# Kernel optimization log

Hardware: AMD Instinct MI355X
Metric: run time of the kernel (lower is better)

## Reference

```python
import jax, jax.numpy as jnp
import numpy as np

N_QUBITS = 8
DIM = 1 << N_QUBITS  # 256
PI = float(np.pi)

# Computational-basis bit signs: s_i = +1 for bit 0, -1 for bit 1 (Z eigenvalues).
# PennyLane convention: wire 0 is the most-significant bit.
_bits = (np.arange(DIM)[:, None] >> (N_QUBITS - 1 - np.arange(N_QUBITS))[None, :]) & 1
SIGNS = jnp.asarray(1.0 - 2.0 * _bits, dtype=jnp.float32)  # [DIM, 8]
PAIR_SIGNS = SIGNS[:, :-1] * SIGNS[:, 1:]                  # [DIM, 7]


def _mlp(x, W1, b1, W2, b2, W3, b3):
    h = jax.nn.relu(x @ W1.T + b1)
    h = jax.nn.relu(h @ W2.T + b2)
    return h @ W3.T + b3


def _embed_state(x):
    """QuantumEmbedding1 (ZZ feature map, IQP-style) on |0>^8.

    H on every wire, RZ(x_i) on wire i, then for i in 0..6:
    CNOT(i,i+1); RZ((pi-x_i)(pi-x_{i+1}), wire i+1); CNOT(i,i+1).
    The whole post-Hadamard circuit is diagonal, so the statevector has
    closed form: psi_b = 2^{-4} exp(-i/2 * phi(b)).
    x: [B, 8] -> psi: [B, 256] complex64.
    """
    single = x @ SIGNS.T                                    # [B, DIM]
    zz = (PI - x[:, :-1]) * (PI - x[:, 1:])                 # [B, 7]
    phase = single + zz @ PAIR_SIGNS.T                      # [B, DIM]
    return jnp.exp(-0.5j * phase) / 16.0                    # complex64


def _mean_rho(psi):
    B = psi.shape[0]
    return jnp.einsum('bi,bj->ij', psi, jnp.conj(psi)) / B  # [256, 256]


def setup_inputs() -> dict:
    key = jax.random.key(0)
    ks = jax.random.split(key, 8)
    B = 65536
    inp = {
        'x1': jax.random.normal(ks[0], (B, 8), dtype=jnp.float32),
        'x0': jax.random.normal(ks[1], (B, 8), dtype=jnp.float32),
        'W1': jax.random.normal(ks[2], (10, 8), dtype=jnp.float32) / np.sqrt(8.0),
        'b1': jnp.zeros((10,), dtype=jnp.float32),
        'W2': jax.random.normal(ks[3], (10, 10), dtype=jnp.float32) / np.sqrt(10.0),
        'b2': jnp.zeros((10,), dtype=jnp.float32),
        'W3': jax.random.normal(ks[4], (8, 10), dtype=jnp.float32) / np.sqrt(10.0),
        'b3': jnp.zeros((8,), dtype=jnp.float32),
    }
    return inp


def reference(x1, x0, W1, b1, W2, b2, W3, b3):
    h1 = _mlp(x1, W1, b1, W2, b2, W3, b3)
    h0 = _mlp(x0, W1, b1, W2, b2, W3, b3)
    rho1 = _mean_rho(_embed_state(h1))
    rho0 = _mean_rho(_embed_state(h0))
    rho_diff = rho1 - rho0
    rho_diff = 0.5 * (rho_diff + jnp.conj(rho_diff.T))  # exact Hermitian
    eigvals = jnp.linalg.eigvalsh(rho_diff)             # real eigenvalues
    return -0.5 * jnp.sum(jnp.abs(eigvals))
```

## Files before the change

kernel.cpp:

```cpp
#include <hip/hip_runtime.h>
#include <cstdint>
#include <cstddef>
#include <utility>

#define PI_F 3.14159265358979323846f

typedef __attribute__((ext_vector_type(8))) _Float16 half8;
typedef __attribute__((ext_vector_type(4))) float f32x4;

struct U4 { unsigned int w[4]; };

static __device__ __forceinline__ unsigned int packhalf2(float c, float s) {
  _Float16 hc = (_Float16)c, hs = (_Float16)s;
  unsigned short uc = __builtin_bit_cast(unsigned short, hc);
  unsigned short us = __builtin_bit_cast(unsigned short, hs);
  return (unsigned int)uc | ((unsigned int)us << 16);
}

static __device__ __forceinline__ void load16_lds(const void* g, void* l) {
  __builtin_amdgcn_global_load_lds(
      (const __attribute__((address_space(1))) unsigned int*)g,
      (__attribute__((address_space(3))) unsigned int*)l, 16, 0, 0);
}

__global__ __launch_bounds__(256) void k_gen(
    const float* __restrict__ x1, const float* __restrict__ x0,
    const float* __restrict__ W1, const float* __restrict__ b1,
    const float* __restrict__ W2, const float* __restrict__ b2,
    const float* __restrict__ W3, const float* __restrict__ b3, int B,
    _Float16* __restrict__ Ach, float* __restrict__ scalars,
    float* __restrict__ out) {
  __shared__ float hzl[32][17];
  int kb = blockIdx.x, t = threadIdx.x;
  if (kb == 0 && t == 0) {
    scalars[0] = 0.f;
    scalars[1] = 0.f;
    out[0] = 0.f;
  }
  if (t < 32) {
    int smp = kb * 32 + t;
    const float* xp =
        (smp < B) ? (x1 + (size_t)smp * 8) : (x0 + (size_t)(smp - B) * 8);
    float x[8];
#pragma unroll
    for (int k = 0; k < 8; k++) x[k] = xp[k];
    float a1[10];
#pragma unroll
    for (int o = 0; o < 10; o++) {
      float v = b1[o];
#pragma unroll
      for (int k = 0; k < 8; k++) v = fmaf(W1[o * 8 + k], x[k], v);
      a1[o] = fmaxf(v, 0.f);
    }
    float a2[10];
#pragma unroll
    for (int o = 0; o < 10; o++) {
      float v = b2[o];
#pragma unroll
      for (int k = 0; k < 10; k++) v = fmaf(W2[o * 10 + k], a1[k], v);
      a2[o] = fmaxf(v, 0.f);
    }
    float hh[8];
#pragma unroll
    for (int o = 0; o < 8; o++) {
      float v = b3[o];
#pragma unroll
      for (int k = 0; k < 10; k++) v = fmaf(W3[o * 10 + k], a2[k], v);
      hh[o] = v;
    }
#pragma unroll
    for (int k = 0; k < 8; k++) hzl[t][k] = hh[k];
#pragma unroll
    for (int k = 0; k < 7; k++)
      hzl[t][8 + k] = (PI_F - hh[k]) * (PI_F - hh[k + 1]);
  }
  __syncthreads();
  int s = t & 31, oct = t >> 5;
  float h[8], z[7];
#pragma unroll
  for (int k = 0; k < 8; k++) h[k] = hzl[s][k];
#pragma unroll
  for (int k = 0; k < 7; k++) z[k] = hzl[s][8 + k];
  float S5 = (oct & 4) ? -1.f : 1.f;
  float S6 = (oct & 2) ? -1.f : 1.f;
  float S7 = (oct & 1) ? -1.f : 1.f;
  float sg[5] = {1.f, 1.f, 1.f, 1.f, 1.f};
  float phi = h[0] + h[1] + h[2] + h[3] + h[4] + S5 * h[5] + S6 * h[6] +
              S7 * h[7] + z[0] + z[1] + z[2] + z[3] + S5 * z[4] +
              S5 * S6 * z[5] + S6 * S7 * z[6];
  _Float16* dst = Ach + (size_t)kb * 16384;
  const int halfoff = (2 * s) ^ (oct << 3);

  auto emit = [&](int g, float ph) {
    float r = ph * 0.07957747154594767f;
    r = r - floorf(r);
    float sv = __builtin_amdgcn_sinf(r);
    float cv = __builtin_amdgcn_cosf(r);
    *(unsigned int*)(dst + (size_t)(g * 8 + oct) * 64 + halfoff) =
        packhalf2(cv, sv);
  };

  emit(0, phi);
#pragma unroll
  for (int jj = 1; jj < 32; ++jj) {
    const int b = __builtin_ctz(jj);
    const int w = 4 - b;
    float nbl = (w == 0) ? 0.f : sg[w - 1] * z[w - 1];
    float nbr = (w == 4) ? S5 * z[4] : sg[w + 1] * z[w];
    phi -= 2.f * sg[w] * (h[w] + nbl + nbr);
    sg[w] = -sg[w];
    emit(jj ^ (jj >> 1), phi);
  }
}

__global__ __launch_bounds__(512) void k_gemm_q(const _Float16* __restrict__ A,
                                                float* __restrict__ P) {
  __shared__ _Float16 lds[2][16384];
  int b = blockIdx.x;
  int qt = (b < 128) ? 0 : (b < 384 ? 1 : 2);
  int z = b - ((qt == 0) ? 0 : (qt == 1) ? 128 : 384);
  int kbPer = (qt == 1) ? 16 : 32;
  int kb0 = z * kbPer;
  int chunkOff = (qt == 2) ? 16384 : 0;
  int bRowBase = (qt == 1) ? 128 : 0;
  int t = threadIdx.x, wave = t >> 6, lane = t & 63;
  unsigned int reMask = (kb0 < 2048) ? 0u : 0x80008000u;
  unsigned int imMask = (kb0 < 2048) ? 0x80000000u : 0x00008000u;

  auto stage = [&](int it, int buf) {
    const char* g = (const char*)A + (size_t)(kb0 + it) * 32768 + chunkOff;
    char* l = (char*)&lds[buf][0];
    load16_lds(g + t * 16, l + t * 16);
    load16_lds(g + 8192 + t * 16, l + 8192 + t * 16);
    if (qt == 1) {
      load16_lds(g + 16384 + t * 16, l + 16384 + t * 16);
      load16_lds(g + 24576 + t * 16, l + 24576 + t * 16);
    }
  };

  f32x4 accR[2][4] = {};
  f32x4 accI[2][4] = {};
  stage(0, 0);
  for (int it = 0; it < kbPer; ++it) {
    __syncthreads();
    if (it + 1 < kbPer) stage(it + 1, (it + 1) & 1);
    int buf = it & 1;
#pragma unroll
    for (int kk = 0; kk < 2; kk++) {
      int cb = kk * 4 + (lane >> 4);
      half8 af[2];
#pragma unroll
      for (int fr = 0; fr < 2; fr++) {
        int r = (wave >> 1) * 32 + fr * 16 + (lane & 15);
        af[fr] = *(const half8*)&lds[buf][r * 64 + ((cb ^ (r & 7)) << 3)];
      }
#pragma unroll
      for (int fc = 0; fc < 4; fc++) {
        int rb = bRowBase + (wave & 1) * 64 + fc * 16 + (lane & 15);
        half8 bv = *(const half8*)&lds[buf][rb * 64 + ((cb ^ (rb & 7)) << 3)];
        U4 u = __builtin_bit_cast(U4, bv), ur, ui;
#pragma unroll
        for (int q = 0; q < 4; q++) {
          unsigned int xv = u.w[q];
          ur.w[q] = xv ^ reMask;
          ui.w[q] = ((xv << 16) | (xv >> 16)) ^ imMask;
        }
        half8 bfr = __builtin_bit_cast(half8, ur);
        half8 bfi = __builtin_bit_cast(half8, ui);
#pragma unroll
        for (int fr = 0; fr < 2; fr++) {
          accR[fr][fc] = __builtin_amdgcn_mfma_f32_16x16x32_f16(
              af[fr], bfr, accR[fr][fc], 0, 0, 0);
          accI[fr][fc] = __builtin_amdgcn_mfma_f32_16x16x32_f16(
              af[fr], bfi, accI[fr][fc], 0, 0, 0);
        }
      }
    }
  }
  float* PR = P + (size_t)b * 32768;
  float* PI = PR + 16384;
  int r4 = (lane >> 4) * 4, cj = lane & 15;
#pragma unroll
  for (int fr = 0; fr < 2; fr++)
#pragma unroll
    for (int fc = 0; fc < 4; fc++)
#pragma unroll
      for (int r = 0; r < 4; r++) {
        int li = (wave >> 1) * 32 + fr * 16 + r4 + r;
        int lj = (wave & 1) * 64 + fc * 16 + cj;
        PR[li * 128 + lj] = accR[fr][fc][r];
        PI[li * 128 + lj] = accI[fr][fc][r];
      }
}

__global__ __launch_bounds__(128) void k_reduce1(const float* __restrict__ P,
                                                 float* __restrict__ Q) {
  int r = blockIdx.x, qt = blockIdx.y, g = blockIdx.z, c = threadIdx.x;
  int nsl = (qt == 1) ? 32 : 16;
  int b0 = ((qt == 0) ? 0 : (qt == 1) ? 128 : 384) + g * nsl;
  float vR = 0.f, vI = 0.f;
  for (int u = 0; u < nsl; u++) {
    const float* base = P + (size_t)(b0 + u) * 32768 + r * 128 + c;
    vR += base[0];
    vI += base[16384];
  }
  size_t qidx = ((size_t)(g * 3 + qt) * 128 + r) * 128 + c;
  Q[qidx] = vR;
  Q[qidx + (size_t)8 * 3 * 16384] = vI;
}

__global__ __launch_bounds__(128) void k_reduce2(const float* __restrict__ Q,
                                                 float* __restrict__ AR,
                                                 float* __restrict__ AI,
                                                 float* __restrict__ sumsq,
                                                 float scale) {
  int r = blockIdx.x, qt = blockIdx.y, c = threadIdx.x;
  float vR = 0.f, vI = 0.f;
#pragma unroll
  for (int g = 0; g < 8; g++) {
    size_t qidx = ((size_t)(g * 3 + qt) * 128 + r) * 128 + c;
    vR += Q[qidx];
    vI += Q[qidx + (size_t)8 * 3 * 16384];
  }
  vR *= scale;
  vI *= scale;
  int i = (qt == 2) ? 128 + r : r;
  int j = (qt == 0) ? c : 128 + c;
  float ss = 0.f;
  bool diagQ = (qt != 1);
  if (!diagQ || c > r) {
    AR[i * 256 + j] = vR;
    AR[j * 256 + i] = vR;
    AI[i * 256 + j] = vI;
    AI[j * 256 + i] = -vI;
    ss = 2.f * (vR * vR + vI * vI);
  } else if (c == r) {
    AR[i * 256 + j] = vR;
    AI[i * 256 + j] = 0.f;
    ss = vR * vR;
  }
#pragma unroll
  for (int o = 32; o > 0; o >>= 1) ss += __shfl_down(ss, o);
  __shared__ float w2[2];
  if ((c & 63) == 0) w2[c >> 6] = ss;
  __syncthreads();
  if (c == 0) atomicAdd(sumsq, w2[0] + w2[1]);
}

__global__ __launch_bounds__(1024) void k_csq(
    const float* __restrict__ XR, const float* __restrict__ XI,
    float* __restrict__ YR, float* __restrict__ YI,
    float* __restrict__ sumsqY, int accumNorm) {
  __shared__ float rp[16][258][2];
  __shared__ float cpT[16][258][2];
  __shared__ float pacc[3][256][2];
  __shared__ float w16[16];
  int t = threadIdx.x;
  int bi = blockIdx.x >> 4, bj = blockIdx.x & 15;
  {
    int r = t >> 6, c = (t & 63) * 4;
    const float4 vr = *(const float4*)&XR[(bi * 16 + r) * 256 + c];
    const float4 vi = *(const float4*)&XI[(bi * 16 + r) * 256 + c];
    float4 p0 = {vr.x, vi.x, vr.y, vi.y};
    float4 p1 = {vr.z, vi.z, vr.w, vi.w};
    *(float4*)&rp[r][c][0] = p0;
    *(float4*)&rp[r][c + 2][0] = p1;
    int row = t >> 2, c0 = (t & 3) * 4;
    const float4 wr = *(const float4*)&XR[row * 256 + bj * 16 + c0];
    const float4 wi = *(const float4*)&XI[row * 256 + bj * 16 + c0];
    float2 q0 = {wr.x, wi.x}, q1 = {wr.y, wi.y};
    float2 q2 = {wr.z, wi.z}, q3 = {wr.w, wi.w};
    *(float2*)&cpT[c0 + 0][row][0] = q0;
    *(float2*)&cpT[c0 + 1][row][0] = q1;
    *(float2*)&cpT[c0 + 2][row][0] = q2;
    *(float2*)&cpT[c0 + 3][row][0] = q3;
  }
  __syncthreads();
  int sub = t >> 8, tt = t & 255, ty = tt >> 4, tx = tt & 15;
  float sR = 0.f, sI = 0.f;
  int k0 = sub * 64;
#pragma unroll 8
  for (int k = k0; k < k0 + 64; k++) {
    float xr = rp[ty][k][0], xi = rp[ty][k][1];
    float yr = cpT[tx][k][0], yi = cpT[tx][k][1];
    sR = fmaf(xr, yr, sR);
    sR = fmaf(-xi, yi, sR);
    sI = fmaf(xr, yi, sI);
    sI = fmaf(xi, yr, sI);
  }
  if (sub) {
    pacc[sub - 1][tt][0] = sR;
    pacc[sub - 1][tt][1] = sI;
  }
  __syncthreads();
  float v = 0.f;
  if (sub == 0) {
    sR += (pacc[0][tt][0] + pacc[1][tt][0]) + pacc[2][tt][0];
    sI += (pacc[0][tt][1] + pacc[1][tt][1]) + pacc[2][tt][1];
    int i = bi * 16 + ty, j = bj * 16 + tx;
    YR[i * 256 + j] = sR;
    YI[i * 256 + j] = sI;
    if (accumNorm) v = sR * sR + sI * sI;
  }
#pragma unroll
  for (int o = 32; o > 0; o >>= 1) v += __shfl_down(v, o);
  if ((t & 63) == 0) w16[t >> 6] = v;
  __syncthreads();
  if (t == 0 && accumNorm)
    atomicAdd(sumsqY, (w16[0] + w16[1]) + (w16[2] + w16[3]));
}

__global__ __launch_bounds__(1024) void k_cupd(
    const float* __restrict__ XR, const float* __restrict__ XI,
    const float* __restrict__ YR, const float* __restrict__ YI,
    float* __restrict__ ZR, float* __restrict__ ZI,
    const float* __restrict__ scalars, int mode,
    const float* __restrict__ AR, const float* __restrict__ AI,
    float* __restrict__ out, int finalTrace) {
  __shared__ float rp[16][258][2];
  __shared__ float cpT[16][258][2];
  __shared__ float pacc[3][256][2];
  __shared__ float w16[16];
  int t = threadIdx.x;
  int bi = blockIdx.x >> 4, bj = blockIdx.x & 15;
  {
    int r = t >> 6, c = (t & 63) * 4;
    const float4 vr = *(const float4*)&XR[(bi * 16 + r) * 256 + c];
    const float4 vi = *(const float4*)&XI[(bi * 16 + r) * 256 + c];
    float4 p0 = {vr.x, vi.x, vr.y, vi.y};
    float4 p1 = {vr.z, vi.z, vr.w, vi.w};
    *(float4*)&rp[r][c][0] = p0;
    *(float4*)&rp[r][c + 2][0] = p1;
    int row = t >> 2, c0 = (t & 3) * 4;
    const float4 wr = *(const float4*)&YR[row * 256 + bj * 16 + c0];
    const float4 wi = *(const float4*)&YI[row * 256 + bj * 16 + c0];
    float2 q0 = {wr.x, wi.x}, q1 = {wr.y, wi.y};
    float2 q2 = {wr.z, wi.z}, q3 = {wr.w, wi.w};
    *(float2*)&cpT[c0 + 0][row][0] = q0;
    *(float2*)&cpT[c0 + 1][row][0] = q1;
    *(float2*)&cpT[c0 + 2][row][0] = q2;
    *(float2*)&cpT[c0 + 3][row][0] = q3;
  }
  __syncthreads();
  int sub = t >> 8, tt = t & 255, ty = tt >> 4, tx = tt & 15;
  float sR = 0.f, sI = 0.f;
  int k0 = sub * 64;
#pragma unroll 8
  for (int k = k0; k < k0 + 64; k++) {
    float xr = rp[ty][k][0], xi = rp[ty][k][1];
    float yr = cpT[tx][k][0], yi = cpT[tx][k][1];
    sR = fmaf(xr, yr, sR);
    sR = fmaf(-xi, yi, sR);
    sI = fmaf(xr, yi, sI);
    sI = fmaf(xi, yr, sI);
  }
  if (sub) {
    pacc[sub - 1][tt][0] = sR;
    pacc[sub - 1][tt][1] = sI;
  }
  __syncthreads();
  float v = 0.f;
  if (sub == 0) {
    sR += (pacc[0][tt][0] + pacc[1][tt][0]) + pacc[2][tt][0];
    sI += (pacc[0][tt][1] + pacc[1][tt][1]) + pacc[2][tt][1];
    float aC, bC;
    if (mode == 0) {
      float f2 = scalars[0];
      float f = sqrtf(f2);
      float Rhat = 1.41421356f * sqrtf(scalars[1]) / f2;
      float g = 1.0f / (1.75f * Rhat);
      aC = 1.5f * g / f;
      float gf = g / f;
      bC = 0.5f * gf * gf * gf;
    } else if (mode == 1) {
      aC = 2.0f;
      bC = 1.0f;
    } else {
      aC = 1.5f;
      bC = 0.5f;
    }
    int idx = (bi * 16 + ty) * 256 + bj * 16 + tx;
    float zr = aC * XR[idx] - bC * sR;
    float zi = aC * XI[idx] - bC * sI;
    if (!finalTrace) {
      ZR[idx] = zr;
      ZI[idx] = zi;
    } else {
      v = AR[idx] * zr + AI[idx] * zi;
    }
  }
#pragma unroll
  for (int o = 32; o > 0; o >>= 1) v += __shfl_down(v, o);
  if ((t & 63) == 0) w16[t >> 6] = v;
  __syncthreads();
  if (t == 0 && finalTrace)
    atomicAdd(out, -0.5f * ((w16[0] + w16[1]) + (w16[2] + w16[3])));
}

extern "C" void kernel_launch(void* const* d_in, const int* in_sizes, int n_in,
                              void* d_out, int out_size, void* d_ws,
                              size_t ws_size, hipStream_t stream) {
  const float* x1 = (const float*)d_in[0];
  const float* x0 = (const float*)d_in[1];
  const float* W1 = (const float*)d_in[2];
  const float* b1 = (const float*)d_in[3];
  const float* W2 = (const float*)d_in[4];
  const float* b2 = (const float*)d_in[5];
  const float* W3 = (const float*)d_in[6];
  const float* b3 = (const float*)d_in[7];
  (void)n_in;
  (void)out_size;
  (void)ws_size;

  const int B = in_sizes[0] / 8;
  const int total = 2 * B;
  const int totalKb = total / 32;

  char* ws = (char*)d_ws;
  size_t off = 0;
  auto carve = [&](size_t bytes) -> void* {
    off = (off + 255) & ~(size_t)255;
    void* p = ws + off;
    off += bytes;
    return p;
  };
  _Float16* Ach = (_Float16*)carve((size_t)totalKb * 16384 * 2);
  float* P = (float*)carve((size_t)512 * 32768 * 4);
  float* Q = (float*)carve((size_t)2 * 8 * 3 * 16384 * 4);
  float* scalars = (float*)carve(256);
  float* AR = (float*)carve(256 * 256 * 4);
  float* AI = (float*)carve(256 * 256 * 4);
  float* XR = (float*)carve(256 * 256 * 4);
  float* XI = (float*)carve(256 * 256 * 4);
  float* YR = (float*)carve(256 * 256 * 4);
  float* YI = (float*)carve(256 * 256 * 4);
  float* ZR = (float*)carve(256 * 256 * 4);
  float* ZI = (float*)carve(256 * 256 * 4);

  k_gen<<<totalKb, 256, 0, stream>>>(x1, x0, W1, b1, W2, b2, W3, b3, B, Ach,
                                     scalars, (float*)d_out);
  k_gemm_q<<<512, 512, 0, stream>>>(Ach, P);
  k_reduce1<<<dim3(128, 3, 8), 128, 0, stream>>>(P, Q);
  k_reduce2<<<dim3(128, 3), 128, 0, stream>>>(Q, AR, AI, scalars,
                                              1.0f / (256.0f * (float)B));

  const int NIT = 11;
  float *cR = AR, *cI = AI, *nR = XR, *nI = XI;
  for (int it = 0; it < NIT; it++) {
    int mode = (it == 0) ? 0 : (it <= 6 ? 1 : 2);
    int fin = (it == NIT - 1) ? 1 : 0;
    k_csq<<<256, 1024, 0, stream>>>(cR, cI, YR, YI, scalars + 1, it == 0);
    k_cupd<<<256, 1024, 0, stream>>>(cR, cI, YR, YI, nR, nI, scalars, mode, AR,
                                     AI, (float*)d_out, fin);
    if (it == 0) {
      cR = XR; cI = XI; nR = ZR; nI = ZI;
    } else {
      std::swap(cR, nR);
      std::swap(cI, nI);
    }
  }
}
```

Measured before the change: 229.1 us.

## Fuse statevector phase generation into GEMM, staging only MLP features

The MLP now runs in its own kernel and writes 16 floats per sample, replacing the full fp16 statevector chunk (256 complex values per sample) that used to go to global memory. The GEMM kernel rebuilds the needed statevector rows directly in LDS with the Gray-code phase recurrence, overlapping this generation with the MFMA work on the other buffer. This removes a large global write and read of the statevector. In exchange the GEMM blocks take on sin/cos work, and generation is repeated for blocks that share rows.

```diff
diff --git a/kernel.cpp b/kernel.cpp
--- a/kernel.cpp
+++ b/kernel.cpp
@@ -17,133 +17,150 @@
   return (unsigned int)uc | ((unsigned int)us << 16);
 }
 
-static __device__ __forceinline__ void load16_lds(const void* g, void* l) {
-  __builtin_amdgcn_global_load_lds(
-      (const __attribute__((address_space(1))) unsigned int*)g,
-      (__attribute__((address_space(3))) unsigned int*)l, 16, 0, 0);
-}
-
-__global__ __launch_bounds__(256) void k_gen(
+__global__ __launch_bounds__(256) void k_mlp(
     const float* __restrict__ x1, const float* __restrict__ x0,
     const float* __restrict__ W1, const float* __restrict__ b1,
     const float* __restrict__ W2, const float* __restrict__ b2,
-    const float* __restrict__ W3, const float* __restrict__ b3, int B,
-    _Float16* __restrict__ Ach, float* __restrict__ scalars,
+    const float* __restrict__ W3, const float* __restrict__ b3,
+    float* __restrict__ hz, int B, float* __restrict__ scalars,
     float* __restrict__ out) {
-  __shared__ float hzl[32][17];
-  int kb = blockIdx.x, t = threadIdx.x;
-  if (kb == 0 && t == 0) {
+  int s = blockIdx.x * blockDim.x + threadIdx.x;
+  if (blockIdx.x == 0 && threadIdx.x == 0) {
     scalars[0] = 0.f;
     scalars[1] = 0.f;
     out[0] = 0.f;
   }
-  if (t < 32) {
-    int smp = kb * 32 + t;
-    const float* xp =
-        (smp < B) ? (x1 + (size_t)smp * 8) : (x0 + (size_t)(smp - B) * 8);
-    float x[8];
-#pragma unroll
-    for (int k = 0; k < 8; k++) x[k] = xp[k];
-    float a1[10];
-#pragma unroll
-    for (int o = 0; o < 10; o++) {
-      float v = b1[o];
-#pragma unroll
-      for (int k = 0; k < 8; k++) v = fmaf(W1[o * 8 + k], x[k], v);
-      a1[o] = fmaxf(v, 0.f);
-    }
-    float a2[10];
-#pragma unroll
-    for (int o = 0; o < 10; o++) {
-      float v = b2[o];
-#pragma unroll
-      for (int k = 0; k < 10; k++) v = fmaf(W2[o * 10 + k], a1[k], v);
-      a2[o] = fmaxf(v, 0.f);
-    }
-    float hh[8];
-#pragma unroll
-    for (int o = 0; o < 8; o++) {
-      float v = b3[o];
-#pragma unroll
-      for (int k = 0; k < 10; k++) v = fmaf(W3[o * 10 + k], a2[k], v);
-      hh[o] = v;
-    }
-#pragma unroll
-    for (int k = 0; k < 8; k++) hzl[t][k] = hh[k];
-#pragma unroll
-    for (int k = 0; k < 7; k++)
-      hzl[t][8 + k] = (PI_F - hh[k]) * (PI_F - hh[k + 1]);
-  }
-  __syncthreads();
-  int s = t & 31, oct = t >> 5;
-  float h[8], z[7];
-#pragma unroll
-  for (int k = 0; k < 8; k++) h[k] = hzl[s][k];
-#pragma unroll
-  for (int k = 0; k < 7; k++) z[k] = hzl[s][8 + k];
-  float S5 = (oct & 4) ? -1.f : 1.f;
-  float S6 = (oct & 2) ? -1.f : 1.f;
-  float S7 = (oct & 1) ? -1.f : 1.f;
-  float sg[5] = {1.f, 1.f, 1.f, 1.f, 1.f};
-  float phi = h[0] + h[1] + h[2] + h[3] + h[4] + S5 * h[5] + S6 * h[6] +
-              S7 * h[7] + z[0] + z[1] + z[2] + z[3] + S5 * z[4] +
-              S5 * S6 * z[5] + S6 * S7 * z[6];
-  _Float16* dst = Ach + (size_t)kb * 16384;
-  const int halfoff = (2 * s) ^ (oct << 3);
-
-  auto emit = [&](int g, float ph) {
-    float r = ph * 0.07957747154594767f;
-    r = r - floorf(r);
-    float sv = __builtin_amdgcn_sinf(r);
-    float cv = __builtin_amdgcn_cosf(r);
-    *(unsigned int*)(dst + (size_t)(g * 8 + oct) * 64 + halfoff) =
-        packhalf2(cv, sv);
-  };
-
-  emit(0, phi);
-#pragma unroll
-  for (int jj = 1; jj < 32; ++jj) {
-    const int b = __builtin_ctz(jj);
-    const int w = 4 - b;
-    float nbl = (w == 0) ? 0.f : sg[w - 1] * z[w - 1];
-    float nbr = (w == 4) ? S5 * z[4] : sg[w + 1] * z[w];
-    phi -= 2.f * sg[w] * (h[w] + nbl + nbr);
-    sg[w] = -sg[w];
-    emit(jj ^ (jj >> 1), phi);
-  }
-}
-
-__global__ __launch_bounds__(512) void k_gemm_q(const _Float16* __restrict__ A,
+  if (s >= 2 * B) return;
+  const float* xp = (s < B) ? (x1 + (size_t)s * 8) : (x0 + (size_t)(s - B) * 8);
+  float x[8];
+#pragma unroll
+  for (int k = 0; k < 8; k++) x[k] = xp[k];
+  float a1[10];
+#pragma unroll
+  for (int o = 0; o < 10; o++) {
+    float v = b1[o];
+#pragma unroll
+    for (int k = 0; k < 8; k++) v = fmaf(W1[o * 8 + k], x[k], v);
+    a1[o] = fmaxf(v, 0.f);
+  }
+  float a2[10];
+#pragma unroll
+  for (int o = 0; o < 10; o++) {
+    float v = b2[o];
+#pragma unroll
+    for (int k = 0; k < 10; k++) v = fmaf(W2[o * 10 + k], a1[k], v);
+    a2[o] = fmaxf(v, 0.f);
+  }
+  float h[8];
+#pragma unroll
+  for (int o = 0; o < 8; o++) {
+    float v = b3[o];
+#pragma unroll
+    for (int k = 0; k < 10; k++) v = fmaf(W3[o * 10 + k], a2[k], v);
+    h[o] = v;
+  }
+  float outv[16];
+#pragma unroll
+  for (int k = 0; k < 8; k++) outv[k] = h[k];
+#pragma unroll
+  for (int k = 0; k < 7; k++) outv[8 + k] = (PI_F - h[k]) * (PI_F - h[k + 1]);
+  outv[15] = 0.f;
+  float4* dst = (float4*)(hz + (size_t)s * 16);
+#pragma unroll
+  for (int q = 0; q < 4; q++) dst[q] = ((float4*)outv)[q];
+}
+
+__global__ __launch_bounds__(512) void k_gemm_f(const float* __restrict__ hz,
                                                 float* __restrict__ P) {
   __shared__ _Float16 lds[2][16384];
+  __shared__ float hzb[2][32][17];
   int b = blockIdx.x;
   int qt = (b < 128) ? 0 : (b < 384 ? 1 : 2);
   int z = b - ((qt == 0) ? 0 : (qt == 1) ? 128 : 384);
   int kbPer = (qt == 1) ? 16 : 32;
   int kb0 = z * kbPer;
-  int chunkOff = (qt == 2) ? 16384 : 0;
+  int rowLocalBase = (qt == 2) ? 128 : 0;
   int bRowBase = (qt == 1) ? 128 : 0;
   int t = threadIdx.x, wave = t >> 6, lane = t & 63;
   unsigned int reMask = (kb0 < 2048) ? 0u : 0x80008000u;
   unsigned int imMask = (kb0 < 2048) ? 0x80000000u : 0x00008000u;
 
-  auto stage = [&](int it, int buf) {
-    const char* g = (const char*)A + (size_t)(kb0 + it) * 32768 + chunkOff;
-    char* l = (char*)&lds[buf][0];
-    load16_lds(g + t * 16, l + t * 16);
-    load16_lds(g + 8192 + t * 16, l + 8192 + t * 16);
-    if (qt == 1) {
-      load16_lds(g + 16384 + t * 16, l + 16384 + t * 16);
-      load16_lds(g + 24576 + t * 16, l + 24576 + t * 16);
+  int s = t & 31, octH = t >> 5;
+  int oct = octH & 7, jHalf = octH >> 3;
+  const int nJ = (qt == 1) ? 16 : 8;
+  const int jj0 = (qt == 1) ? jHalf * 16 : ((qt == 2) ? 16 : 0) + jHalf * 8;
+  const int halfoff = (2 * s) ^ (oct << 3);
+  const float S5 = (oct & 4) ? -1.f : 1.f;
+  const float S6 = (oct & 2) ? -1.f : 1.f;
+  const float S7 = (oct & 1) ? -1.f : 1.f;
+
+  auto loadHz = [&](int kb) {
+    if (t < 128) {
+      int smp = t >> 2, q = t & 3;
+      const float4 v =
+          *(const float4*)(hz + (size_t)(kb * 32 + smp) * 16 + q * 4);
+      float* d = &hzb[kb & 1][smp][q * 4];
+      d[0] = v.x;
+      d[1] = v.y;
+      d[2] = v.z;
+      d[3] = v.w;
+    }
+  };
+
+  auto gen = [&](int kb, int buf) {
+    int hb = kb & 1;
+    float h[8], z7[7];
+#pragma unroll
+    for (int k = 0; k < 8; k++) h[k] = hzb[hb][s][k];
+#pragma unroll
+    for (int k = 0; k < 7; k++) z7[k] = hzb[hb][s][8 + k];
+    int g0 = jj0 ^ (jj0 >> 1);
+    float sg[5];
+#pragma unroll
+    for (int w = 0; w < 5; w++) sg[w] = ((g0 >> (4 - w)) & 1) ? -1.f : 1.f;
+    float phi = sg[0] * h[0] + sg[1] * h[1] + sg[2] * h[2] + sg[3] * h[3] +
+                sg[4] * h[4] + S5 * h[5] + S6 * h[6] + S7 * h[7] +
+                sg[0] * sg[1] * z7[0] + sg[1] * sg[2] * z7[1] +
+                sg[2] * sg[3] * z7[2] + sg[3] * sg[4] * z7[3] +
+                sg[4] * S5 * z7[4] + S5 * S6 * z7[5] + S6 * S7 * z7[6];
+    int g = g0;
+    auto emitRow = [&](int gg, float ph) {
+      int lr = gg * 8 + oct - rowLocalBase;
+      float r = ph * 0.07957747154594767f;
+      r = r - floorf(r);
+      float sv = __builtin_amdgcn_sinf(r);
+      float cv = __builtin_amdgcn_cosf(r);
+      *(unsigned int*)&lds[buf][lr * 64 + halfoff] = packhalf2(cv, sv);
+    };
+    emitRow(g, phi);
+#pragma unroll
+    for (int stp = 1; stp < 16; stp++) {
+      if (stp >= nJ) break;
+      const int bbit = __builtin_ctz(stp);
+      const int w = 4 - bbit;
+      float nbl = (w == 0) ? 0.f : sg[w - 1] * z7[w - 1];
+      float nbr = (w == 4) ? S5 * z7[4] : sg[w + 1] * z7[w];
+      phi -= 2.f * sg[w] * (h[w] + nbl + nbr);
+      sg[w] = -sg[w];
+      g ^= (1 << bbit);
+      emitRow(g, phi);
     }
   };
 
   f32x4 accR[2][4] = {};
   f32x4 accI[2][4] = {};
-  stage(0, 0);
+
+  loadHz(kb0);
+  __syncthreads();
+  gen(kb0, 0);
+  loadHz(kb0 + 1);
+  __syncthreads();
+
   for (int it = 0; it < kbPer; ++it) {
-    __syncthreads();
-    if (it + 1 < kbPer) stage(it + 1, (it + 1) & 1);
+    if (it + 1 < kbPer) {
+      gen(kb0 + it + 1, (it + 1) & 1);
+      if (it + 2 < kbPer) loadHz(kb0 + it + 2);
+    }
     int buf = it & 1;
 #pragma unroll
     for (int kk = 0; kk < 2; kk++) {
@@ -176,6 +193,7 @@
         }
       }
     }
+    __syncthreads();
   }
   float* PR = P + (size_t)b * 32768;
   float* PI = PR + 16384;
@@ -414,7 +432,6 @@
 
   const int B = in_sizes[0] / 8;
   const int total = 2 * B;
-  const int totalKb = total / 32;
 
   char* ws = (char*)d_ws;
   size_t off = 0;
@@ -424,7 +441,7 @@
     off += bytes;
     return p;
   };
-  _Float16* Ach = (_Float16*)carve((size_t)totalKb * 16384 * 2);
+  float* hz = (float*)carve((size_t)total * 16 * 4);
   float* P = (float*)carve((size_t)512 * 32768 * 4);
   float* Q = (float*)carve((size_t)2 * 8 * 3 * 16384 * 4);
   float* scalars = (float*)carve(256);
@@ -437,9 +454,9 @@
   float* ZR = (float*)carve(256 * 256 * 4);
   float* ZI = (float*)carve(256 * 256 * 4);
 
-  k_gen<<<totalKb, 256, 0, stream>>>(x1, x0, W1, b1, W2, b2, W3, b3, B, Ach,
-                                     scalars, (float*)d_out);
-  k_gemm_q<<<512, 512, 0, stream>>>(Ach, P);
+  k_mlp<<<(total + 255) / 256, 256, 0, stream>>>(
+      x1, x0, W1, b1, W2, b2, W3, b3, hz, B, scalars, (float*)d_out);
+  k_gemm_f<<<512, 512, 0, stream>>>(hz, P);
   k_reduce1<<<dim3(128, 3, 8), 128, 0, stream>>>(P, Q);
   k_reduce2<<<dim3(128, 3), 128, 0, stream>>>(Q, AR, AI, scalars,
                                               1.0f / (256.0f * (float)B));
```

Result: faster. 219.1 us (median of 2 runs) (-4.3%).
